# Optimization experiments

Measured on AMD Instinct MI355X. Metric: run time of the kernel, lower is better.

Reference implementation:

```python
import jax, jax.numpy as jnp
import numpy as np

B, T, D, H, V, L = 2, 1024, 512, 8, 50257, 4
HD = D // H  # head size
FF = 4 * D


def _ln(x, w, b):
    mu = jnp.mean(x, axis=-1, keepdims=True)
    var = jnp.mean((x - mu) ** 2, axis=-1, keepdims=True)
    return (x - mu) * jax.lax.rsqrt(var + 1e-5) * w + b


def setup_inputs() -> dict:
    key = jax.random.key(0)
    ks = jax.random.split(key, 12)
    s = 0.02
    return {
        "idx": jax.random.randint(ks[0], (B, T), 0, V),
        "tok_emb": jax.random.normal(ks[1], (V, D)) * s,
        "pos_emb": jax.random.normal(ks[2], (T, D)) * s,
        "Wq": jax.random.normal(ks[3], (L, H, D, HD)) * s,
        "Wk": jax.random.normal(ks[4], (L, H, D, HD)) * s,
        "Wv": jax.random.normal(ks[5], (L, H, D, HD)) * s,
        "Wo": jax.random.normal(ks[6], (L, D, D)) * s,
        "bo": jnp.zeros((L, D)),
        "W1": jax.random.normal(ks[7], (L, D, FF)) * s,
        "b1": jnp.zeros((L, FF)),
        "W2": jax.random.normal(ks[8], (L, FF, D)) * s,
        "b2": jnp.zeros((L, D)),
        "ln1_w": jnp.ones((L, D)), "ln1_b": jnp.zeros((L, D)),
        "ln2_w": jnp.ones((L, D)), "ln2_b": jnp.zeros((L, D)),
        "Wlm": jax.random.normal(ks[9], (D, V)) * s,
        "blm": jnp.zeros((V,)),
    }


def reference(idx, tok_emb, pos_emb, Wq, Wk, Wv, Wo, bo, W1, b1, W2, b2,
              ln1_w, ln1_b, ln2_w, ln2_b, Wlm, blm):
    b, t = idx.shape
    x = tok_emb[idx] + pos_emb[:t]  # [B,T,D]
    mask = jnp.tril(jnp.ones((t, t), dtype=bool))
    scale = D ** (-0.5)  # NOTE: original scales by full n_embd, not head_size
    for l in range(L):
        # pre-norm that also feeds the residual (x = ln1(x); x = x + sa(x))
        h = _ln(x, ln1_w[l], ln1_b[l])
        q = jnp.einsum('btd,hdk->bhtk', h, Wq[l])
        k = jnp.einsum('btd,hdk->bhtk', h, Wk[l])
        v = jnp.einsum('btd,hdk->bhtk', h, Wv[l])
        wei = jnp.einsum('bhtk,bhsk->bhts', q, k) * scale
        wei = jnp.where(mask, wei, -jnp.inf)
        wei = jax.nn.softmax(wei, axis=-1)  # dropout omitted (eval mode)
        att = jnp.einsum('bhts,bhsk->bhtk', wei, v)
        att = att.transpose(0, 2, 1, 3).reshape(b, t, D)  # concat heads
        x = h + att @ Wo[l] + bo[l]
        h2 = _ln(x, ln2_w[l], ln2_b[l])
        x = h2 + jax.nn.relu(h2 @ W1[l] + b1[l]) @ W2[l] + b2[l]
    logits = x @ Wlm + blm  # [B,T,V]
    return logits
```

## Files before the change

### kernel.cpp

```cpp
#include <hip/hip_runtime.h>
#include <hip/hip_bf16.h>

typedef __hip_bfloat16 bf16;
typedef __attribute__((ext_vector_type(8))) short s8v;
typedef __attribute__((ext_vector_type(4))) float f4v;

#define B_ 2
#define T_ 1024
#define D_ 512
#define H_ 8
#define HD_ 64
#define V_ 50257
#define VPAD_ 51200
#define L_ 4
#define FF_ 2048
#define BT_ (B_*T_)

__device__ __forceinline__ float ldw(const void* p, size_t i, int f32m) {
  return f32m ? ((const float*)p)[i] : __bfloat162float(((const bf16*)p)[i]);
}

__device__ __forceinline__ void gload_lds16(const void* g, void* l) {
  __builtin_amdgcn_global_load_lds((const __attribute__((address_space(1))) void*)g,
                                   (__attribute__((address_space(3))) void*)l, 16, 0, 0);
}

__global__ void detect_kernel(const void* __restrict__ ln1w, int* __restrict__ flag) {
  unsigned u = *(const unsigned*)ln1w;
  *flag = (u == 0x3F800000u) ? 1 : 0;
}

__global__ void embed_kernel(const int* __restrict__ idx, const void* __restrict__ tok,
                             const void* __restrict__ pos, float* __restrict__ x,
                             const int* __restrict__ flag) {
  int f32m = *flag;
  int i = blockIdx.x * 256 + threadIdx.x;
  int bt = i >> 9;
  int d  = i & (D_ - 1);
  int t  = bt & (T_ - 1);
  int tk = idx[bt];
  x[i] = ldw(tok, (size_t)tk * D_ + d, f32m) + ldw(pos, (size_t)t * D_ + d, f32m);
}

__global__ void ln_kernel(const float* __restrict__ x, const void* __restrict__ w,
                          const void* __restrict__ b, size_t eoff,
                          bf16* __restrict__ hb, float* __restrict__ hf,
                          const int* __restrict__ flag) {
  int f32m = *flag;
  int t = blockIdx.x;
  int tid = threadIdx.x;
  const float* row = x + (size_t)t * D_;
  float v0 = row[tid], v1 = row[tid + 256];
  __shared__ float red[256];
  red[tid] = v0 + v1;
  __syncthreads();
  for (int s = 128; s > 0; s >>= 1) { if (tid < s) red[tid] += red[tid + s]; __syncthreads(); }
  float mu = red[0] * (1.f / D_);
  __syncthreads();
  float d0 = v0 - mu, d1 = v1 - mu;
  red[tid] = d0 * d0 + d1 * d1;
  __syncthreads();
  for (int s = 128; s > 0; s >>= 1) { if (tid < s) red[tid] += red[tid + s]; __syncthreads(); }
  float rs = rsqrtf(red[0] * (1.f / D_) + 1e-5f);
  float o0 = d0 * rs * ldw(w, eoff + tid, f32m)       + ldw(b, eoff + tid, f32m);
  float o1 = d1 * rs * ldw(w, eoff + tid + 256, f32m) + ldw(b, eoff + tid + 256, f32m);
  size_t base = (size_t)t * D_;
  hf[base + tid] = o0;        hf[base + tid + 256] = o1;
  hb[base + tid] = __float2bfloat16(o0);
  hb[base + tid + 256] = __float2bfloat16(o1);
}

__global__ void repack_qkv_all_kernel(const void* __restrict__ Wq, const void* __restrict__ Wk,
                                      const void* __restrict__ Wv, bf16* __restrict__ out,
                                      const int* __restrict__ flag) {
  int f32m = *flag;
  int zz = blockIdx.z;
  size_t eoff = (size_t)zz * H_ * D_ * HD_;
  out += (size_t)zz * 1536 * 512;
  int i = blockIdx.x * 256 + threadIdx.x;
  int n = i >> 9, k = i & 511;
  int sel = n >> 9; int cc = n & 511; int hh = cc >> 6; int hd = cc & 63;
  const void* src = (sel == 0) ? Wq : (sel == 1) ? Wk : Wv;
  out[i] = __float2bfloat16(ldw(src, eoff + ((size_t)hh * D_ + k) * HD_ + hd, f32m));
}

__global__ void repack_qkv_kernel(const void* __restrict__ Wq, const void* __restrict__ Wk,
                                  const void* __restrict__ Wv, size_t eoff,
                                  bf16* __restrict__ out, const int* __restrict__ flag) {
  int f32m = *flag;
  int i = blockIdx.x * 256 + threadIdx.x;
  int n = i >> 9, k = i & 511;
  int sel = n >> 9; int cc = n & 511; int hh = cc >> 6; int hd = cc & 63;
  const void* src = (sel == 0) ? Wq : (sel == 1) ? Wk : Wv;
  out[i] = __float2bfloat16(ldw(src, eoff + ((size_t)hh * D_ + k) * HD_ + hd, f32m));
}

__global__ void transpose_kernel(const void* __restrict__ in, size_t eoff,
                                 bf16* __restrict__ out, int K, int Nin,
                                 const int* __restrict__ flag) {
  int f32m = *flag;
  __shared__ bf16 tl[32][33];
  int n0 = blockIdx.x * 32, k0 = blockIdx.y * 32;
  int tx = threadIdx.x & 31, ty = threadIdx.x >> 5;
#pragma unroll
  for (int i = 0; i < 4; ++i) {
    int k = k0 + ty + i * 8;
    int n = n0 + tx;
    float v = (n < Nin) ? ldw(in, eoff + (size_t)k * Nin + n, f32m) : 0.f;
    tl[ty + i * 8][tx] = __float2bfloat16(v);
  }
  __syncthreads();
#pragma unroll
  for (int i = 0; i < 4; ++i) {
    int n = n0 + ty + i * 8;
    out[(size_t)n * K + k0 + tx] = tl[tx][ty + i * 8];
  }
}

__global__ void transpose_all_kernel(const void* __restrict__ in,
                                     bf16* __restrict__ out,
                                     int K, int Nin, const int* __restrict__ flag) {
  int f32m = *flag;
  int zz = blockIdx.z;
  size_t eoff = (size_t)zz * K * Nin;
  out += (size_t)zz * Nin * K;
  __shared__ bf16 tl[32][33];
  int n0 = blockIdx.x * 32, k0 = blockIdx.y * 32;
  int tx = threadIdx.x & 31, ty = threadIdx.x >> 5;
#pragma unroll
  for (int i = 0; i < 4; ++i) {
    int k = k0 + ty + i * 8;
    int n = n0 + tx;
    tl[ty + i * 8][tx] = __float2bfloat16(ldw(in, eoff + (size_t)k * Nin + n, f32m));
  }
  __syncthreads();
#pragma unroll
  for (int i = 0; i < 4; ++i) {
    int n = n0 + ty + i * 8;
    out[(size_t)n * K + k0 + tx] = tl[tx][ty + i * 8];
  }
}

template<int OUTM, int BIAS, int RES, int RELU, int XB>
__global__ __launch_bounds__(256)
void mfma_gemm64(const bf16* __restrict__ A, const bf16* __restrict__ Bt,
                 void* __restrict__ Cout, const void* __restrict__ bias, size_t bieoff,
                 const float* __restrict__ res, bf16* __restrict__ xb2,
                 const int* __restrict__ flag, int M, int Nc, int K) {
  __shared__ __align__(16) short As[2][2048];
  __shared__ __align__(16) short Bs[2][2048];
  const int tid = threadIdx.x;
  const int brow = blockIdx.x * 64;
  const int bcol = blockIdx.y * 64;
  const int w = tid >> 6, lane = tid & 63;
  const int wr = w >> 1, wc = w & 1;
  const int lr = lane & 15, lk = lane >> 4;

  const int e0 = tid * 8;
  const int r0 = e0 >> 5;
  const int c0 = (e0 & 31) ^ ((r0 & 3) << 3);
  const bf16* ag0 = A + (size_t)(brow + r0) * K + c0;
  const bf16* bg0 = Bt + (size_t)(bcol + r0) * K + c0;

  int aoff[2], boff[2];
#pragma unroll
  for (int i = 0; i < 2; ++i) {
    int ra = wr * 32 + i * 16 + lr;
    aoff[i] = ra * 32 + ((lk * 8) ^ ((lr & 3) << 3));
    int rb = wc * 32 + i * 16 + lr;
    boff[i] = rb * 32 + ((lk * 8) ^ ((lr & 3) << 3));
  }

  f4v acc[2][2];
  const f4v z = {0.f, 0.f, 0.f, 0.f};
#pragma unroll
  for (int i = 0; i < 2; ++i)
#pragma unroll
    for (int j = 0; j < 2; ++j) acc[i][j] = z;

  const int nt = K >> 5;
  gload_lds16(ag0, &As[0][e0]);
  gload_lds16(bg0, &Bs[0][e0]);

  for (int kt = 0; kt < nt; ++kt) {
    __syncthreads();
    const int cur = kt & 1;
    if (kt + 1 < nt) {
      const size_t ko = (size_t)(kt + 1) * 32;
      gload_lds16(ag0 + ko, &As[cur ^ 1][e0]);
      gload_lds16(bg0 + ko, &Bs[cur ^ 1][e0]);
    }
    s8v a[2], b[2];
#pragma unroll
    for (int i = 0; i < 2; ++i) a[i] = *(const s8v*)&As[cur][aoff[i]];
#pragma unroll
    for (int i = 0; i < 2; ++i) b[i] = *(const s8v*)&Bs[cur][boff[i]];
#pragma unroll
    for (int mi = 0; mi < 2; ++mi)
#pragma unroll
      for (int ni = 0; ni < 2; ++ni)
        acc[mi][ni] = __builtin_amdgcn_mfma_f32_16x16x32_bf16(a[mi], b[ni], acc[mi][ni], 0, 0, 0);
  }

  const int f32m = *flag;
#pragma unroll
  for (int mi = 0; mi < 2; ++mi) {
    const int row = brow + wr * 32 + mi * 16 + lk * 4;
#pragma unroll
    for (int ni = 0; ni < 2; ++ni) {
      const int col = bcol + wc * 32 + ni * 16 + lr;
      if (col < Nc) {
        float bv = BIAS ? ldw(bias, bieoff + col, f32m) : 0.f;
#pragma unroll
        for (int rr = 0; rr < 4; ++rr) {
          float v = acc[mi][ni][rr] + bv;
          size_t ci = (size_t)(row + rr) * Nc + col;
          if (RES) v += res[ci];
          if (RELU) v = fmaxf(v, 0.f);
          if (OUTM == 0) ((float*)Cout)[ci] = v;
          else           ((bf16*)Cout)[ci] = __float2bfloat16(v);
          if (XB) xb2[ci] = __float2bfloat16(v);
        }
      }
    }
  }
}

__global__ __launch_bounds__(512, 1)
void mfma_gemm_lm256(const bf16* __restrict__ A, const bf16* __restrict__ Bt,
                     void* __restrict__ Cout, const void* __restrict__ bias,
                     const int* __restrict__ flag, int M, int Nc) {
  const int K = 512;
  __shared__ __align__(16) short As[4][8192];
  __shared__ __align__(16) short Bs[4][8192];
  const int bid = blockIdx.x;
  const int xcd = bid & 7;
  const int chunk = bid >> 3;
  const int brow = (chunk & 7) * 256;
  const int bcol = (xcd * 25 + (chunk >> 3)) * 256;
  const int tid = threadIdx.x;
  const int w = tid >> 6, lane = tid & 63;
  const int wr = w >> 2, wc = w & 3;
  const int lr = lane & 15, lk = lane >> 4;

  const int e0 = tid * 8, e1 = 4096 + tid * 8;
  const int r0 = e0 >> 5, r1 = e1 >> 5;
  const int c0 = (e0 & 31) ^ (((r0 >> 1) & 3) << 3);
  const int c1 = (e1 & 31) ^ (((r1 >> 1) & 3) << 3);
  const bf16* ag0 = A + (size_t)(brow + r0) * K + c0;
  const bf16* ag1 = A + (size_t)(brow + r1) * K + c1;
  const bf16* bg0 = Bt + (size_t)(bcol + r0) * K + c0;
  const bf16* bg1 = Bt + (size_t)(bcol + r1) * K + c1;

  int aoff[8], boff[4];
#pragma unroll
  for (int mi = 0; mi < 8; ++mi) {
    int ra = wr * 128 + mi * 16 + lr;
    aoff[mi] = ra * 32 + ((lk * 8) ^ (((ra >> 1) & 3) << 3));
  }
#pragma unroll
  for (int ni = 0; ni < 4; ++ni) {
    int rb = wc * 64 + ni * 16 + lr;
    boff[ni] = rb * 32 + ((lk * 8) ^ (((rb >> 1) & 3) << 3));
  }

  f4v acc[8][4];
  const f4v z = {0.f, 0.f, 0.f, 0.f};
#pragma unroll
  for (int i = 0; i < 8; ++i)
#pragma unroll
    for (int j = 0; j < 4; ++j) acc[i][j] = z;

#pragma unroll
  for (int t = 0; t < 3; ++t) {
    const size_t ko = (size_t)t * 32;
    gload_lds16(ag0 + ko, &As[t][e0]); gload_lds16(ag1 + ko, &As[t][e1]);
    gload_lds16(bg0 + ko, &Bs[t][e0]); gload_lds16(bg1 + ko, &Bs[t][e1]);
  }

#define LM_MFMA_PAIR(P, A0, A1)                                                     \
    acc[2*(P)][0]   = __builtin_amdgcn_mfma_f32_16x16x32_bf16(A0, b0, acc[2*(P)][0], 0, 0, 0);   \
    acc[2*(P)][1]   = __builtin_amdgcn_mfma_f32_16x16x32_bf16(A0, b1, acc[2*(P)][1], 0, 0, 0);   \
    acc[2*(P)][2]   = __builtin_amdgcn_mfma_f32_16x16x32_bf16(A0, b2, acc[2*(P)][2], 0, 0, 0);   \
    acc[2*(P)][3]   = __builtin_amdgcn_mfma_f32_16x16x32_bf16(A0, b3, acc[2*(P)][3], 0, 0, 0);   \
    acc[2*(P)+1][0] = __builtin_amdgcn_mfma_f32_16x16x32_bf16(A1, b0, acc[2*(P)+1][0], 0, 0, 0); \
    acc[2*(P)+1][1] = __builtin_amdgcn_mfma_f32_16x16x32_bf16(A1, b1, acc[2*(P)+1][1], 0, 0, 0); \
    acc[2*(P)+1][2] = __builtin_amdgcn_mfma_f32_16x16x32_bf16(A1, b2, acc[2*(P)+1][2], 0, 0, 0); \
    acc[2*(P)+1][3] = __builtin_amdgcn_mfma_f32_16x16x32_bf16(A1, b3, acc[2*(P)+1][3], 0, 0, 0)

  for (int kt = 0; kt < 16; ++kt) {
    const int cur = kt & 3;
    const int nb = (kt + 3) & 3;
    const size_t ko = (size_t)(kt + 3) * 32;
    const bool pf = (kt + 3 < 16);

    if (kt < 14)       asm volatile("s_waitcnt vmcnt(8)" ::: "memory");
    else if (kt == 14) asm volatile("s_waitcnt vmcnt(4)" ::: "memory");
    else               asm volatile("s_waitcnt vmcnt(0)" ::: "memory");
    __builtin_amdgcn_s_barrier();
    s8v b0 = *(const s8v*)&Bs[cur][boff[0]];
    s8v b1 = *(const s8v*)&Bs[cur][boff[1]];
    s8v b2 = *(const s8v*)&Bs[cur][boff[2]];
    s8v b3 = *(const s8v*)&Bs[cur][boff[3]];
    s8v a0 = *(const s8v*)&As[cur][aoff[0]];
    s8v a1 = *(const s8v*)&As[cur][aoff[1]];
    if (pf) gload_lds16(ag0 + ko, &As[nb][e0]);
    asm volatile("s_waitcnt lgkmcnt(0)" ::: "memory");
    __builtin_amdgcn_sched_barrier(0);
    __builtin_amdgcn_s_setprio(1);
    LM_MFMA_PAIR(0, a0, a1);
    __builtin_amdgcn_s_setprio(0);
    __builtin_amdgcn_s_barrier();

    a0 = *(const s8v*)&As[cur][aoff[2]];
    a1 = *(const s8v*)&As[cur][aoff[3]];
    if (pf) gload_lds16(ag1 + ko, &As[nb][e1]);
    __builtin_amdgcn_s_barrier();
    asm volatile("s_waitcnt lgkmcnt(0)" ::: "memory");
    __builtin_amdgcn_sched_barrier(0);
    __builtin_amdgcn_s_setprio(1);
    LM_MFMA_PAIR(1, a0, a1);
    __builtin_amdgcn_s_setprio(0);
    __builtin_amdgcn_s_barrier();

    a0 = *(const s8v*)&As[cur][aoff[4]];
    a1 = *(const s8v*)&As[cur][aoff[5]];
    if (pf) gload_lds16(bg0 + ko, &Bs[nb][e0]);
    __builtin_amdgcn_s_barrier();
    asm volatile("s_waitcnt lgkmcnt(0)" ::: "memory");
    __builtin_amdgcn_sched_barrier(0);
    __builtin_amdgcn_s_setprio(1);
    LM_MFMA_PAIR(2, a0, a1);
    __builtin_amdgcn_s_setprio(0);
    __builtin_amdgcn_s_barrier();

    a0 = *(const s8v*)&As[cur][aoff[6]];
    a1 = *(const s8v*)&As[cur][aoff[7]];
    if (pf) gload_lds16(bg1 + ko, &Bs[nb][e1]);
    __builtin_amdgcn_s_barrier();
    asm volatile("s_waitcnt lgkmcnt(0)" ::: "memory");
    __builtin_amdgcn_sched_barrier(0);
    __builtin_amdgcn_s_setprio(1);
    LM_MFMA_PAIR(3, a0, a1);
    __builtin_amdgcn_s_setprio(0);
    __builtin_amdgcn_s_barrier();
  }
#undef LM_MFMA_PAIR

  const int f32m = *flag;
#pragma unroll
  for (int mi = 0; mi < 8; ++mi) {
    const int row = brow + wr * 128 + mi * 16 + lk * 4;
#pragma unroll
    for (int ni = 0; ni < 4; ++ni) {
      const int col = bcol + wc * 64 + ni * 16 + lr;
      if (col < Nc) {
        float bv = ldw(bias, col, f32m);
#pragma unroll
        for (int rr = 0; rr < 4; ++rr) {
          float v = acc[mi][ni][rr] + bv;
          size_t ci = (size_t)(row + rr) * Nc + col;
          if (f32m) ((float*)Cout)[ci] = v;
          else      ((bf16*)Cout)[ci] = __float2bfloat16(v);
        }
      }
    }
  }
}

#define ATT_SCALE 0.044194173824159216f
__global__ __launch_bounds__(128) void fattn_kernel(const bf16* __restrict__ qkv,
                                                    bf16* __restrict__ att) {
  const int tid = threadIdx.x;
  const int w = tid >> 6, lane = tid & 63;
  const int lr = lane & 15, lk = lane >> 4;
  const int sx = blockIdx.x;
  const int strip = (sx & 1) ? (31 - (sx >> 1)) : (sx >> 1);
  const int s0 = strip * 32;
  const int hh = blockIdx.y, b = blockIdx.z;
  const int q0w = s0 + w * 16;

  __shared__ __align__(16) short Klds[64 * 64];
  __shared__ __align__(16) short Vt[64 * 72];
  __shared__ __align__(16) short Pl[2][16 * 72];
  unsigned* vt32 = (unsigned*)Vt;

  const bf16* qbase = qkv + (size_t)(b * T_ + q0w + lr) * 1536 + hh * 64;
  s8v qf[2];
#pragma unroll
  for (int kk = 0; kk < 2; ++kk)
    qf[kk] = *(const s8v*)(qbase + kk * 32 + lk * 8);

  const bf16* kg = qkv + (size_t)b * T_ * 1536 + 512 + hh * 64;
  const bf16* vg = kg + 512;

  f4v acc_o[4];
  const f4v z4 = {0.f, 0.f, 0.f, 0.f};
#pragma unroll
  for (int dt = 0; dt < 4; ++dt) acc_o[dt] = z4;
  float m[4], l[4];
#pragma unroll
  for (int r = 0; r < 4; ++r) { m[r] = -1e30f; l[r] = 0.f; }

  const int jmax = (s0 + 31) >> 6;
  for (int jt = 0; jt <= jmax; ++jt) {
    __syncthreads();
    const bf16* kt = kg + (size_t)jt * 64 * 1536;
#pragma unroll
    for (int c = 0; c < 4; ++c) {
      int e = tid * 8 + c * 1024;
      int row = e >> 6, col = e & 63;
      int colw = col ^ ((row & 7) << 3);
      gload_lds16(kt + (size_t)row * 1536 + colw, &Klds[e]);
    }
    const bf16* vgt = vg + (size_t)jt * 64 * 1536;
#pragma unroll
    for (int u = 0; u < 2; ++u) {
      int unit = tid * 2 + u;
      int kp = unit >> 3, cc = (unit & 7) * 8;
      s8v v0 = *(const s8v*)(vgt + (size_t)(2 * kp) * 1536 + cc);
      s8v v1 = *(const s8v*)(vgt + (size_t)(2 * kp + 1) * 1536 + cc);
#pragma unroll
      for (int j = 0; j < 8; ++j) {
        unsigned pk = (unsigned)(unsigned short)v0[j] |
                      ((unsigned)(unsigned short)v1[j] << 16);
        vt32[(cc + j) * 36 + kp] = pk;
      }
    }
    __syncthreads();

    if (jt * 64 <= q0w + 15) {
      const bool diag = (jt == jmax);
      f4v s[4];
#pragma unroll
      for (int nt = 0; nt < 4; ++nt) s[nt] = z4;
#pragma unroll
      for (int kk = 0; kk < 2; ++kk)
#pragma unroll
        for (int nt = 0; nt < 4; ++nt) {
          int row = nt * 16 + lr;
          const s8v kf = *(const s8v*)&Klds[row * 64 +
                           ((kk * 32 + lk * 8) ^ ((lr & 7) << 3))];
          s[nt] = __builtin_amdgcn_mfma_f32_16x16x32_bf16(qf[kk], kf, s[nt], 0, 0, 0);
        }
      float pv[4][4];
#pragma unroll
      for (int nt = 0; nt < 4; ++nt)
#pragma unroll
        for (int r = 0; r < 4; ++r) {
          float v = s[nt][r] * ATT_SCALE;
          if (diag && (jt * 64 + nt * 16 + lr > q0w + lk * 4 + r)) v = -1e30f;
          pv[nt][r] = v;
        }
#pragma unroll
      for (int r = 0; r < 4; ++r) {
        float mm = fmaxf(fmaxf(pv[0][r], pv[1][r]), fmaxf(pv[2][r], pv[3][r]));
        mm = fmaxf(mm, __shfl_xor(mm, 1));
        mm = fmaxf(mm, __shfl_xor(mm, 2));
        mm = fmaxf(mm, __shfl_xor(mm, 4));
        mm = fmaxf(mm, __shfl_xor(mm, 8));
        float nm = fmaxf(m[r], mm);
        float cf = __expf(m[r] - nm);
        m[r] = nm;
        float ls = 0.f;
#pragma unroll
        for (int nt = 0; nt < 4; ++nt) {
          float p = __expf(pv[nt][r] - nm);
          pv[nt][r] = p;
          ls += p;
        }
        ls += __shfl_xor(ls, 1); ls += __shfl_xor(ls, 2);
        ls += __shfl_xor(ls, 4); ls += __shfl_xor(ls, 8);
        l[r] = l[r] * cf + ls;
#pragma unroll
        for (int dt = 0; dt < 4; ++dt) acc_o[dt][r] *= cf;
      }
      bf16* pw = (bf16*)&Pl[w][0];
#pragma unroll
      for (int nt = 0; nt < 4; ++nt)
#pragma unroll
        for (int r = 0; r < 4; ++r)
          pw[(lk * 4 + r) * 72 + nt * 16 + lr] = __float2bfloat16(pv[nt][r]);
#pragma unroll
      for (int kk = 0; kk < 2; ++kk) {
        const s8v pa = *(const s8v*)&Pl[w][lr * 72 + kk * 32 + lk * 8];
#pragma unroll
        for (int dt = 0; dt < 4; ++dt) {
          const s8v vf = *(const s8v*)&Vt[(dt * 16 + lr) * 72 + kk * 32 + lk * 8];
          acc_o[dt] = __builtin_amdgcn_mfma_f32_16x16x32_bf16(pa, vf, acc_o[dt], 0, 0, 0);
        }
      }
    }
  }

#pragma unroll
  for (int dt = 0; dt < 4; ++dt)
#pragma unroll
    for (int r = 0; r < 4; ++r) {
      int q = q0w + lk * 4 + r;
      float v = acc_o[dt][r] / l[r];
      att[(size_t)(b * T_ + q) * D_ + hh * 64 + dt * 16 + lr] = __float2bfloat16(v);
    }
}

__global__ void cast_kernel(const float* __restrict__ x, bf16* __restrict__ xb) {
  int i = blockIdx.x * 256 + threadIdx.x;
  xb[i] = __float2bfloat16(x[i]);
}

__global__ void lm_fallback_kernel(const float* __restrict__ A, const void* __restrict__ Bw,
                                   void* __restrict__ Cout, const void* __restrict__ bias,
                                   const int* __restrict__ flag, int M, int N, int K) {
  const int f32m = *flag;
  __shared__ __align__(16) float As[16][72];
  __shared__ __align__(16) float Bs[16][72];
  const int tid = threadIdx.x;
  const int brow = blockIdx.y * 64;
  const int bcol = blockIdx.x * 64;
  const int tr = tid >> 4, tc = tid & 15;
  float acc[4][4] = {};
  for (int k0 = 0; k0 < K; k0 += 16) {
#pragma unroll
    for (int i = 0; i < 4; ++i) {
      int e = tid + i * 256;
      int r = e >> 4, c = e & 15;
      As[c][r] = A[(size_t)(brow + r) * K + k0 + c];
    }
#pragma unroll
    for (int i = 0; i < 4; ++i) {
      int e = tid + i * 256;
      int r = e >> 6, c = e & 63;
      int col = bcol + c;
      Bs[r][c] = (col < N) ? ldw(Bw, (size_t)(k0 + r) * N + col, f32m) : 0.f;
    }
    __syncthreads();
#pragma unroll
    for (int kk = 0; kk < 16; ++kk) {
      const float4 av = *reinterpret_cast<const float4*>(&As[kk][tr * 4]);
      const float4 bv = *reinterpret_cast<const float4*>(&Bs[kk][tc * 4]);
      float a_[4] = {av.x, av.y, av.z, av.w};
      float b_[4] = {bv.x, bv.y, bv.z, bv.w};
#pragma unroll
      for (int i = 0; i < 4; ++i)
#pragma unroll
        for (int j = 0; j < 4; ++j) acc[i][j] += a_[i] * b_[j];
    }
    __syncthreads();
  }
#pragma unroll
  for (int i = 0; i < 4; ++i) {
    int row = brow + tr * 4 + i;
#pragma unroll
    for (int j = 0; j < 4; ++j) {
      int col = bcol + tc * 4 + j;
      if (col < N) {
        float v = acc[i][j] + ldw(bias, col, f32m);
        if (f32m) ((float*)Cout)[(size_t)row * N + col] = v;
        else      ((bf16*) Cout)[(size_t)row * N + col] = __float2bfloat16(v);
      }
    }
  }
}

template<int OUTM, int BI, int RE, int RL, int XB>
static void launch_g64(const bf16* A, const bf16* Bt, void* C, const void* bias,
                       size_t bieoff, const float* res, bf16* xb2, const int* flag,
                       int M, int Nc, int Npad, int K, hipStream_t s) {
  dim3 grid(M / 64, Npad / 64);
  mfma_gemm64<OUTM, BI, RE, RL, XB><<<grid, 256, 0, s>>>(A, Bt, C, bias, bieoff, res,
                                                         xb2, flag, M, Nc, K);
}

extern "C" void kernel_launch(void* const* d_in, const int* in_sizes, int n_in,
                              void* d_out, int out_size, void* d_ws, size_t ws_size,
                              hipStream_t stream) {
  const int*  idx  = (const int*) d_in[0];
  const void* tok  = d_in[1];
  const void* pos  = d_in[2];
  const void* Wq   = d_in[3];
  const void* Wk   = d_in[4];
  const void* Wv   = d_in[5];
  const void* Wo   = d_in[6];
  const void* bo   = d_in[7];
  const void* W1   = d_in[8];
  const void* b1   = d_in[9];
  const void* W2   = d_in[10];
  const void* b2   = d_in[11];
  const void* ln1w = d_in[12];
  const void* ln1b = d_in[13];
  const void* ln2w = d_in[14];
  const void* ln2b = d_in[15];
  const void* Wlm  = d_in[16];
  const void* blm  = d_in[17];

  char* p = (char*)d_ws;
  int*   flag = (int*)p;            p += 256;
  float* x    = (float*)p;          p += (size_t)BT_ * D_ * 4;
  float* hf   = (float*)p;          p += (size_t)BT_ * D_ * 4;
  bf16*  h    = (bf16*)p;           p += (size_t)BT_ * D_ * 2;
  bf16*  R    = (bf16*)p;           p += (size_t)BT_ * FF_ * 2;
  bf16*  qkvP = (bf16*)p;           p += (size_t)L_ * 1536 * 512 * 2;
  bf16*  woP  = (bf16*)p;           p += (size_t)L_ * 512 * 512 * 2;
  bf16*  w1P  = (bf16*)p;           p += (size_t)L_ * 2048 * 512 * 2;
  bf16*  w2P  = (bf16*)p;           p += (size_t)L_ * 512 * 2048 * 2;
  bf16*  wlmP = (bf16*)p;
  size_t need_all = (size_t)(p - (char*)d_ws) + (size_t)VPAD_ * D_ * 2;
  bf16*  wrep = qkvP;
  bf16*  wlmF = (bf16*)((char*)qkvP + (size_t)FF_ * D_ * 2);
  size_t need_old = ((char*)wlmF - (char*)d_ws) + (size_t)VPAD_ * D_ * 2;

  bf16* qkv = R;
  bf16* att = R + (size_t)BT_ * 1536;
  bf16* ff  = R;
  bf16* xb  = h;

  detect_kernel<<<1, 1, 0, stream>>>(ln1w, flag);
  embed_kernel<<<BT_ * D_ / 256, 256, 0, stream>>>(idx, tok, pos, x, flag);

  if (ws_size >= need_all) {
    repack_qkv_all_kernel<<<dim3(1536 * 512 / 256, 1, L_), 256, 0, stream>>>(
        Wq, Wk, Wv, qkvP, flag);
    transpose_all_kernel<<<dim3(16, 16, L_), 256, 0, stream>>>(Wo, woP, 512, 512, flag);
    transpose_all_kernel<<<dim3(64, 16, L_), 256, 0, stream>>>(W1, w1P, 512, 2048, flag);
    transpose_all_kernel<<<dim3(16, 64, L_), 256, 0, stream>>>(W2, w2P, 2048, 512, flag);
    transpose_kernel<<<dim3(VPAD_ / 32, 16), 256, 0, stream>>>(Wlm, 0, wlmP, 512, V_, flag);

    for (int l = 0; l < L_; ++l) {
      ln_kernel<<<BT_, 256, 0, stream>>>(x, ln1w, ln1b, (size_t)l * D_, h, hf, flag);
      launch_g64<1,0,0,0,0>(h, qkvP + (size_t)l * 1536 * 512, qkv, nullptr, 0, nullptr,
                            nullptr, flag, BT_, 1536, 1536, 512, stream);
      fattn_kernel<<<dim3(32, H_, B_), 128, 0, stream>>>(qkv, att);
      launch_g64<0,1,1,0,0>(att, woP + (size_t)l * 512 * 512, x, bo, (size_t)l * D_, hf,
                            nullptr, flag, BT_, 512, 512, 512, stream);
      ln_kernel<<<BT_, 256, 0, stream>>>(x, ln2w, ln2b, (size_t)l * D_, h, hf, flag);
      launch_g64<1,1,0,1,0>(h, w1P + (size_t)l * 2048 * 512, ff, b1, (size_t)l * FF_,
                            nullptr, nullptr, flag, BT_, 2048, 2048, 512, stream);
      if (l < L_ - 1)
        launch_g64<0,1,1,0,0>(ff, w2P + (size_t)l * 512 * 2048, x, b2, (size_t)l * D_, hf,
                              nullptr, flag, BT_, 512, 512, 2048, stream);
      else
        launch_g64<0,1,1,0,1>(ff, w2P + (size_t)l * 512 * 2048, x, b2, (size_t)l * D_, hf,
                              xb, flag, BT_, 512, 512, 2048, stream);
    }
    mfma_gemm_lm256<<<(BT_ / 256) * (VPAD_ / 256), 512, 0, stream>>>(
        xb, wlmP, d_out, blm, flag, BT_, V_);
  } else {
    const bool big = ws_size >= need_old;
    for (int l = 0; l < L_; ++l) {
      ln_kernel<<<BT_, 256, 0, stream>>>(x, ln1w, ln1b, (size_t)l * D_, h, hf, flag);
      repack_qkv_kernel<<<1536 * 512 / 256, 256, 0, stream>>>(
          Wq, Wk, Wv, (size_t)l * H_ * D_ * HD_, wrep, flag);
      launch_g64<1,0,0,0,0>(h, wrep, qkv, nullptr, 0, nullptr, nullptr, flag,
                            BT_, 1536, 1536, 512, stream);
      fattn_kernel<<<dim3(32, H_, B_), 128, 0, stream>>>(qkv, att);
      transpose_kernel<<<dim3(16, 16), 256, 0, stream>>>(Wo, (size_t)l * D_ * D_, wrep, 512, 512, flag);
      launch_g64<0,1,1,0,0>(att, wrep, x, bo, (size_t)l * D_, hf, nullptr, flag,
                            BT_, 512, 512, 512, stream);
      ln_kernel<<<BT_, 256, 0, stream>>>(x, ln2w, ln2b, (size_t)l * D_, h, hf, flag);
      transpose_kernel<<<dim3(64, 16), 256, 0, stream>>>(W1, (size_t)l * D_ * FF_, wrep, 512, 2048, flag);
      launch_g64<1,1,0,1,0>(h, wrep, ff, b1, (size_t)l * FF_, nullptr, nullptr, flag,
                            BT_, 2048, 2048, 512, stream);
      transpose_kernel<<<dim3(16, 64), 256, 0, stream>>>(W2, (size_t)l * FF_ * D_, wrep, 2048, 512, flag);
      launch_g64<0,1,1,0,0>(ff, wrep, x, b2, (size_t)l * D_, hf, nullptr, flag,
                            BT_, 512, 512, 2048, stream);
    }
    if (big) {
      cast_kernel<<<BT_ * D_ / 256, 256, 0, stream>>>(x, xb);
      transpose_kernel<<<dim3(VPAD_ / 32, 16), 256, 0, stream>>>(Wlm, 0, wlmF, 512, V_, flag);
      mfma_gemm_lm256<<<(BT_ / 256) * (VPAD_ / 256), 512, 0, stream>>>(
          xb, wlmF, d_out, blm, flag, BT_, V_);
    } else {
      lm_fallback_kernel<<<dim3((V_ + 63) / 64, BT_ / 64), 256, 0, stream>>>(
          x, Wlm, d_out, blm, flag, BT_, V_, 512);
    }
  }
}
```

Measured before the change: 768.0 us.

## Use 128x128 MFMA GEMM tiles for QKV/FFN1 and warp-per-row layernorm

Adds a 128x128-tile MFMA GEMM (4 waves, each computing a 64x64 sub-tile, double-buffered LDS loads via global_load_lds) and uses it for the QKV and FFN-up projections, which raises operand reuse per LDS load compared with the 64x64 kernel. It also rewrites layernorm so that one wavefront handles one row, with float4 vector loads and shuffle reductions in place of the shared-memory tree reduction and its repeated barriers. The larger tiles mean fewer blocks (e.g. 16x12 for QKV), which may underfill the GPU's compute units, and the GEMM uses more registers per thread.

```diff
diff --git a/kernel.cpp b/kernel.cpp
--- a/kernel.cpp
+++ b/kernel.cpp
@@ -47,27 +47,34 @@
                           bf16* __restrict__ hb, float* __restrict__ hf,
                           const int* __restrict__ flag) {
   int f32m = *flag;
-  int t = blockIdx.x;
-  int tid = threadIdx.x;
-  const float* row = x + (size_t)t * D_;
-  float v0 = row[tid], v1 = row[tid + 256];
-  __shared__ float red[256];
-  red[tid] = v0 + v1;
-  __syncthreads();
-  for (int s = 128; s > 0; s >>= 1) { if (tid < s) red[tid] += red[tid + s]; __syncthreads(); }
-  float mu = red[0] * (1.f / D_);
-  __syncthreads();
-  float d0 = v0 - mu, d1 = v1 - mu;
-  red[tid] = d0 * d0 + d1 * d1;
-  __syncthreads();
-  for (int s = 128; s > 0; s >>= 1) { if (tid < s) red[tid] += red[tid + s]; __syncthreads(); }
-  float rs = rsqrtf(red[0] * (1.f / D_) + 1e-5f);
-  float o0 = d0 * rs * ldw(w, eoff + tid, f32m)       + ldw(b, eoff + tid, f32m);
-  float o1 = d1 * rs * ldw(w, eoff + tid + 256, f32m) + ldw(b, eoff + tid + 256, f32m);
-  size_t base = (size_t)t * D_;
-  hf[base + tid] = o0;        hf[base + tid + 256] = o1;
-  hb[base + tid] = __float2bfloat16(o0);
-  hb[base + tid + 256] = __float2bfloat16(o1);
+  int wv = threadIdx.x >> 6, lane = threadIdx.x & 63;
+  int t = blockIdx.x * 4 + wv;
+  const float* row = x + (size_t)t * D_ + lane * 8;
+  float4 v0 = *(const float4*)row;
+  float4 v1 = *(const float4*)(row + 4);
+  float sum = v0.x + v0.y + v0.z + v0.w + v1.x + v1.y + v1.z + v1.w;
+#pragma unroll
+  for (int off = 32; off > 0; off >>= 1) sum += __shfl_xor(sum, off);
+  float mu = sum * (1.f / D_);
+  float d[8] = {v0.x - mu, v0.y - mu, v0.z - mu, v0.w - mu,
+                v1.x - mu, v1.y - mu, v1.z - mu, v1.w - mu};
+  float s2 = 0.f;
+#pragma unroll
+  for (int j = 0; j < 8; ++j) s2 += d[j] * d[j];
+#pragma unroll
+  for (int off = 32; off > 0; off >>= 1) s2 += __shfl_xor(s2, off);
+  float rs = rsqrtf(s2 * (1.f / D_) + 1e-5f);
+  size_t base = (size_t)t * D_ + lane * 8;
+  float o[8];
+  s8v hb8;
+#pragma unroll
+  for (int j = 0; j < 8; ++j) {
+    o[j] = d[j] * rs * ldw(w, eoff + lane * 8 + j, f32m) + ldw(b, eoff + lane * 8 + j, f32m);
+    ((bf16*)&hb8)[j] = __float2bfloat16(o[j]);
+  }
+  *(float4*)(hf + base)     = make_float4(o[0], o[1], o[2], o[3]);
+  *(float4*)(hf + base + 4) = make_float4(o[4], o[5], o[6], o[7]);
+  *(s8v*)(hb + base) = hb8;
 }
 
 __global__ void repack_qkv_all_kernel(const void* __restrict__ Wq, const void* __restrict__ Wk,
@@ -220,6 +227,95 @@
           if (OUTM == 0) ((float*)Cout)[ci] = v;
           else           ((bf16*)Cout)[ci] = __float2bfloat16(v);
           if (XB) xb2[ci] = __float2bfloat16(v);
+        }
+      }
+    }
+  }
+}
+
+template<int OUTM, int BIAS, int RES, int RELU>
+__global__ __launch_bounds__(256)
+void mfma_gemm128(const bf16* __restrict__ A, const bf16* __restrict__ Bt,
+                  void* __restrict__ Cout, const void* __restrict__ bias, size_t bieoff,
+                  const float* __restrict__ res, const int* __restrict__ flag,
+                  int M, int Nc, int K) {
+  __shared__ __align__(16) short As[2][4096];
+  __shared__ __align__(16) short Bs[2][4096];
+  const int tid = threadIdx.x;
+  const int brow = blockIdx.x * 128;
+  const int bcol = blockIdx.y * 128;
+  const int w = tid >> 6, lane = tid & 63;
+  const int wr = w >> 1, wc = w & 1;
+  const int lr = lane & 15, lk = lane >> 4;
+
+  const int e0 = tid * 8, e1 = 2048 + tid * 8;
+  const int r0 = e0 >> 5, r1 = e1 >> 5;
+  const int c0 = (e0 & 31) ^ ((r0 & 3) << 3);
+  const int c1 = (e1 & 31) ^ ((r1 & 3) << 3);
+  const bf16* ag0 = A + (size_t)(brow + r0) * K + c0;
+  const bf16* ag1 = A + (size_t)(brow + r1) * K + c1;
+  const bf16* bg0 = Bt + (size_t)(bcol + r0) * K + c0;
+  const bf16* bg1 = Bt + (size_t)(bcol + r1) * K + c1;
+
+  int aoff[4], boff[4];
+#pragma unroll
+  for (int i = 0; i < 4; ++i) {
+    int ra = wr * 64 + i * 16 + lr;
+    aoff[i] = ra * 32 + ((lk * 8) ^ ((lr & 3) << 3));
+    int rb = wc * 64 + i * 16 + lr;
+    boff[i] = rb * 32 + ((lk * 8) ^ ((lr & 3) << 3));
+  }
+
+  f4v acc[4][4];
+  const f4v z = {0.f, 0.f, 0.f, 0.f};
+#pragma unroll
+  for (int i = 0; i < 4; ++i)
+#pragma unroll
+    for (int j = 0; j < 4; ++j) acc[i][j] = z;
+
+  const int nt = K >> 5;
+  gload_lds16(ag0, &As[0][e0]); gload_lds16(ag1, &As[0][e1]);
+  gload_lds16(bg0, &Bs[0][e0]); gload_lds16(bg1, &Bs[0][e1]);
+
+  for (int kt = 0; kt < nt; ++kt) {
+    __syncthreads();
+    const int cur = kt & 1;
+    if (kt + 1 < nt) {
+      const size_t ko = (size_t)(kt + 1) * 32;
+      gload_lds16(ag0 + ko, &As[cur ^ 1][e0]);
+      gload_lds16(ag1 + ko, &As[cur ^ 1][e1]);
+      gload_lds16(bg0 + ko, &Bs[cur ^ 1][e0]);
+      gload_lds16(bg1 + ko, &Bs[cur ^ 1][e1]);
+    }
+    s8v a[4], b[4];
+#pragma unroll
+    for (int i = 0; i < 4; ++i) a[i] = *(const s8v*)&As[cur][aoff[i]];
+#pragma unroll
+    for (int i = 0; i < 4; ++i) b[i] = *(const s8v*)&Bs[cur][boff[i]];
+#pragma unroll
+    for (int mi = 0; mi < 4; ++mi)
+#pragma unroll
+      for (int ni = 0; ni < 4; ++ni)
+        acc[mi][ni] = __builtin_amdgcn_mfma_f32_16x16x32_bf16(a[mi], b[ni], acc[mi][ni], 0, 0, 0);
+  }
+
+  const int f32m = *flag;
+#pragma unroll
+  for (int mi = 0; mi < 4; ++mi) {
+    const int row = brow + wr * 64 + mi * 16 + lk * 4;
+#pragma unroll
+    for (int ni = 0; ni < 4; ++ni) {
+      const int col = bcol + wc * 64 + ni * 16 + lr;
+      if (col < Nc) {
+        float bv = BIAS ? ldw(bias, bieoff + col, f32m) : 0.f;
+#pragma unroll
+        for (int rr = 0; rr < 4; ++rr) {
+          float v = acc[mi][ni][rr] + bv;
+          size_t ci = (size_t)(row + rr) * Nc + col;
+          if (RES) v += res[ci];
+          if (RELU) v = fmaxf(v, 0.f);
+          if (OUTM == 0) ((float*)Cout)[ci] = v;
+          else           ((bf16*)Cout)[ci] = __float2bfloat16(v);
         }
       }
     }
@@ -569,6 +665,15 @@
   dim3 grid(M / 64, Npad / 64);
   mfma_gemm64<OUTM, BI, RE, RL, XB><<<grid, 256, 0, s>>>(A, Bt, C, bias, bieoff, res,
                                                          xb2, flag, M, Nc, K);
+}
+
+template<int OUTM, int BI, int RE, int RL>
+static void launch_g128(const bf16* A, const bf16* Bt, void* C, const void* bias,
+                        size_t bieoff, const float* res, const int* flag,
+                        int M, int Nc, int Npad, int K, hipStream_t s) {
+  dim3 grid(M / 128, Npad / 128);
+  mfma_gemm128<OUTM, BI, RE, RL><<<grid, 256, 0, s>>>(A, Bt, C, bias, bieoff, res,
+                                                      flag, M, Nc, K);
 }
 
 extern "C" void kernel_launch(void* const* d_in, const int* in_sizes, int n_in,
@@ -626,15 +731,15 @@
     transpose_kernel<<<dim3(VPAD_ / 32, 16), 256, 0, stream>>>(Wlm, 0, wlmP, 512, V_, flag);
 
     for (int l = 0; l < L_; ++l) {
-      ln_kernel<<<BT_, 256, 0, stream>>>(x, ln1w, ln1b, (size_t)l * D_, h, hf, flag);
-      launch_g64<1,0,0,0,0>(h, qkvP + (size_t)l * 1536 * 512, qkv, nullptr, 0, nullptr,
-                            nullptr, flag, BT_, 1536, 1536, 512, stream);
+      ln_kernel<<<BT_ / 4, 256, 0, stream>>>(x, ln1w, ln1b, (size_t)l * D_, h, hf, flag);
+      launch_g128<1,0,0,0>(h, qkvP + (size_t)l * 1536 * 512, qkv, nullptr, 0, nullptr,
+                           flag, BT_, 1536, 1536, 512, stream);
       fattn_kernel<<<dim3(32, H_, B_), 128, 0, stream>>>(qkv, att);
       launch_g64<0,1,1,0,0>(att, woP + (size_t)l * 512 * 512, x, bo, (size_t)l * D_, hf,
                             nullptr, flag, BT_, 512, 512, 512, stream);
-      ln_kernel<<<BT_, 256, 0, stream>>>(x, ln2w, ln2b, (size_t)l * D_, h, hf, flag);
-      launch_g64<1,1,0,1,0>(h, w1P + (size_t)l * 2048 * 512, ff, b1, (size_t)l * FF_,
-                            nullptr, nullptr, flag, BT_, 2048, 2048, 512, stream);
+      ln_kernel<<<BT_ / 4, 256, 0, stream>>>(x, ln2w, ln2b, (size_t)l * D_, h, hf, flag);
+      launch_g128<1,1,0,1>(h, w1P + (size_t)l * 2048 * 512, ff, b1, (size_t)l * FF_,
+                           nullptr, flag, BT_, 2048, 2048, 512, stream);
       if (l < L_ - 1)
         launch_g64<0,1,1,0,0>(ff, w2P + (size_t)l * 512 * 2048, x, b2, (size_t)l * D_, hf,
                               nullptr, flag, BT_, 512, 512, 2048, stream);
@@ -647,7 +752,7 @@
   } else {
     const bool big = ws_size >= need_old;
     for (int l = 0; l < L_; ++l) {
-      ln_kernel<<<BT_, 256, 0, stream>>>(x, ln1w, ln1b, (size_t)l * D_, h, hf, flag);
+      ln_kernel<<<BT_ / 4, 256, 0, stream>>>(x, ln1w, ln1b, (size_t)l * D_, h, hf, flag);
       repack_qkv_kernel<<<1536 * 512 / 256, 256, 0, stream>>>(
           Wq, Wk, Wv, (size_t)l * H_ * D_ * HD_, wrep, flag);
       launch_g64<1,0,0,0,0>(h, wrep, qkv, nullptr, 0, nullptr, nullptr, flag,
@@ -656,7 +761,7 @@
       transpose_kernel<<<dim3(16, 16), 256, 0, stream>>>(Wo, (size_t)l * D_ * D_, wrep, 512, 512, flag);
       launch_g64<0,1,1,0,0>(att, wrep, x, bo, (size_t)l * D_, hf, nullptr, flag,
                             BT_, 512, 512, 512, stream);
-      ln_kernel<<<BT_, 256, 0, stream>>>(x, ln2w, ln2b, (size_t)l * D_, h, hf, flag);
+      ln_kernel<<<BT_ / 4, 256, 0, stream>>>(x, ln2w, ln2b, (size_t)l * D_, h, hf, flag);
       transpose_kernel<<<dim3(64, 16), 256, 0, stream>>>(W1, (size_t)l * D_ * FF_, wrep, 512, 2048, flag);
       launch_g64<1,1,0,1,0>(h, wrep, ff, b1, (size_t)l * FF_, nullptr, nullptr, flag,
                             BT_, 2048, 2048, 512, stream);
```

Result: slower. 817.7 us (median of 2 runs) (+6.5%).
